# Performance work log

Measured on AMD Instinct MI355X. Metric: run time of the kernel, lower is better.

## Reference

```python
import jax, jax.numpy as jnp
import numpy as np

B, NQ, NK, C = 16, 8, 4096, 256
H = W = 64
HEADS = 8
CI = 128          # embedding_dim // attention_downsample_rate
HD = CI // HEADS  # per-head dim
EPS = float(np.finfo(np.float32).tiny)


def _gumbel_topk(scores, noise, n):
    # iterative gumbel-softmax top-k relaxation with straight-through hard k-hot
    g = scores + noise
    khot = jnp.zeros_like(g)
    onehot = jnp.zeros_like(g)
    for _ in range(n):
        g = g + jnp.log(jnp.maximum(1.0 - onehot, EPS))
        onehot = jax.nn.softmax(g, axis=-1)
        khot = khot + onehot
    _, ind = jax.lax.top_k(khot, n)
    rows = jnp.arange(khot.shape[0])[:, None]
    hard = jnp.zeros_like(khot).at[rows, ind].set(1.0)
    ret = hard - jax.lax.stop_gradient(khot) + khot  # == hard numerically
    return ret, jnp.sort(ind, axis=1)  # sorted idx = row-major order of boolean-mask select


def _sample_points(pe, content, ret, idx):
    # pe [H,W,C], content [b,H,W,C], ret [b,HW] k-hot, idx [b,k] sorted
    b = ret.shape[0]
    m = ret.reshape(b, H, W, 1)
    pe_m = (pe[None] * m).reshape(b, H * W, -1)
    c_m = (content * m).reshape(b, H * W, -1)
    take = lambda a: jnp.take_along_axis(a, idx[:, :, None], axis=1)
    return take(pe_m), take(c_m)


def _mlp(x, W1, b1, W2, b2, W3, b3):
    x = jax.nn.relu(x @ W1 + b1)
    x = jax.nn.relu(x @ W2 + b2)
    return x @ W3 + b3


def _forward(queries, keys, query_pe, key_pe, guiding_embedding, gumbel_p, gumbel_n,
             static_uncertain, static_refined, Wq, bq, Wk, bk, Wv, bv, Wo, bo,
             uW1, ub1, uW2, ub2, uW3, ub3, rW1, rb1, rW2, rb2, rW3, rb3,
             pe_gauss, point_pos, point_neg, n_sample_points):
    b = queries.shape[0]
    g = guiding_embedding.reshape(b, C, H * W).transpose(0, 2, 1)  # [b, HW, C]
    g = g * keys  # elementwise gating -> new guiding embedding

    # cross attention token -> image (internal dim CI, HEADS heads)
    def split_heads(x, Wx, bx):
        return (x @ Wx + bx).reshape(b, -1, HEADS, HD).transpose(0, 2, 1, 3)
    qh = split_heads(queries + query_pe, Wq, bq)
    kh = split_heads(g + key_pe, Wk, bk)
    vh = split_heads(g, Wv, bv)
    attn = jax.nn.softmax(jnp.einsum('bhqd,bhkd->bhqk', qh, kh) / np.float32(np.sqrt(HD)), axis=-1)
    out = jnp.einsum('bhqk,bhkd->bhqd', attn, vh).transpose(0, 2, 1, 3).reshape(b, -1, CI)
    queries = out @ Wo + bo  # [b, NQ, C]

    q1 = queries[:, 1, :]
    unc_tok = _mlp(jnp.concatenate([jnp.broadcast_to(static_uncertain, (b, C)), q1], -1),
                   uW1, ub1, uW2, ub2, uW3, ub3)
    ref_tok = _mlp(jnp.concatenate([jnp.broadcast_to(static_refined, (b, C)), q1], -1),
                   rW1, rb1, rW2, rb2, rW3, rb3)

    img = g.transpose(0, 2, 1)  # [b, C, HW]
    unc_norm = jax.nn.sigmoid(jnp.einsum('bc,bcn->bn', unc_tok, img))
    ref_mask = jnp.einsum('bc,bcn->bn', ref_tok, img)
    coarse_mask = jnp.einsum('bc,bcn->bn', q1, img)

    queries = jnp.concatenate([queries[:, 0:1], ref_tok[:, None, :], queries[:, 2:]], axis=1)

    # point-sampling reference map + gumbel-softmax top-k (training-path math)
    ref_map = unc_norm * (jax.nn.sigmoid(ref_mask) - jax.nn.sigmoid(coarse_mask))  # [b, HW]
    ret_p, idx_p = _gumbel_topk(ref_map, gumbel_p, n_sample_points)
    ret_n, idx_n = _gumbel_topk(-ref_map, gumbel_n, n_sample_points)

    # random fourier positional encoding of the 64x64 grid (SAM PositionEmbeddingRandom)
    xs = (jnp.arange(W, dtype=jnp.float32) + 0.5) / W
    ys = (jnp.arange(H, dtype=jnp.float32) + 0.5) / H
    coords = jnp.stack([jnp.tile(xs[None, :], (H, 1)), jnp.tile(ys[:, None], (1, W))], axis=-1)
    proj = ((2.0 * coords - 1.0) @ pe_gauss) * np.float32(2.0 * np.pi)  # [H, W, C//2]
    pe = jnp.concatenate([jnp.sin(proj), jnp.cos(proj)], axis=-1)       # [H, W, C]

    # F.interpolate of a 64x64 map to (64,64) is the identity here
    content = (keys + g).reshape(b, H, W, C)

    sp_pe, sp_c = _sample_points(pe, content, ret_p, idx_p)
    sn_pe, sn_c = _sample_points(pe, content, ret_n, idx_n)
    sp_pe = sp_pe + point_pos  # prompt_encoder.point_embeddings[1]
    sn_pe = sn_pe + point_neg  # prompt_encoder.point_embeddings[0]

    query_pe = jnp.concatenate([query_pe, sp_pe, sn_pe], axis=1)
    queries = jnp.concatenate([queries, sp_c, sn_c], axis=1)
    # pack (queries, query_pe) into one array for a single-output reference
    return jnp.concatenate([queries, query_pe], axis=1)  # [b, 2*(NQ+2k), C]


def setup_inputs():
    key = jax.random.key(0)
    ks = iter(jax.random.split(key, 48))
    n = lambda shape, s=1.0: jax.random.normal(next(ks), shape, jnp.float32) * s
    z = lambda shape: jnp.zeros(shape, jnp.float32)
    return {
        'queries': n((B, NQ, C)),
        'keys': n((B, NK, C)),
        'query_pe': n((B, NQ, C)),
        'key_pe': n((B, NK, C)),
        'guiding_embedding': n((B, C, H, W)),
        'gumbel_p': jax.random.gumbel(next(ks), (B, NK), jnp.float32),
        'gumbel_n': jax.random.gumbel(next(ks), (B, NK), jnp.float32),
        'static_uncertain': n((C,), 0.02),
        'static_refined': n((C,), 0.02),
        'Wq': n((C, CI), 0.02), 'bq': z((CI,)),
        'Wk': n((C, CI), 0.02), 'bk': z((CI,)),
        'Wv': n((C, CI), 0.02), 'bv': z((CI,)),
        'Wo': n((CI, C), 0.02), 'bo': z((C,)),
        'uW1': n((2 * C, C // 4), 0.05), 'ub1': z((C // 4,)),
        'uW2': n((C // 4, C // 4), 0.05), 'ub2': z((C // 4,)),
        'uW3': n((C // 4, C), 0.05), 'ub3': z((C,)),
        'rW1': n((2 * C, C // 4), 0.05), 'rb1': z((C // 4,)),
        'rW2': n((C // 4, C // 4), 0.05), 'rb2': z((C // 4,)),
        'rW3': n((C // 4, C), 0.05), 'rb3': z((C,)),
        'pe_gauss': n((2, C // 2)),
        'point_pos': n((C,), 0.02),
        'point_neg': n((C,), 0.02),
        'n_sample_points': 4,
    }


def reference(queries, keys, query_pe, key_pe, guiding_embedding, gumbel_p, gumbel_n,
              static_uncertain, static_refined, Wq, bq, Wk, bk, Wv, bv, Wo, bo,
              uW1, ub1, uW2, ub2, uW3, ub3, rW1, rb1, rW2, rb2, rW3, rb3,
              pe_gauss, point_pos, point_neg, n_sample_points):
    return _forward(queries, keys, query_pe, key_pe, guiding_embedding, gumbel_p, gumbel_n,
                    static_uncertain, static_refined, Wq, bq, Wk, bk, Wv, bv, Wo, bo,
                    uW1, ub1, uW2, ub2, uW3, ub3, rW1, rb1, rW2, rb2, rW3, rb3,
                    pe_gauss, point_pos, point_neg, n_sample_points)
```

## Files before the change

### kernel.cpp

```cpp
#include <hip/hip_runtime.h>

#define BB 16
#define NQn 8
#define NK 4096
#define CC 256
#define NHEADS 8
#define CIn 128
#define HDn 16
#define NHQ 64
#define EPS_TINY 1.17549435e-38f

constexpr size_t OFF_QK   = 0;
constexpr size_t OFF_QBK  = OFF_QK  + (size_t)BB*CC*NHQ;
constexpr size_t OFF_SC   = OFF_QBK + (size_t)BB*NHQ;
constexpr size_t OFF_MP   = OFF_SC  + (size_t)BB*NK*NHQ;
constexpr size_t OFF_SP   = OFF_MP  + (size_t)BB*64*NHQ;
constexpr size_t OFF_M    = OFF_SP  + (size_t)BB*64*NHQ;
constexpr size_t OFF_RS   = OFF_M   + (size_t)BB*NHQ;
constexpr size_t OFF_AVP  = OFF_RS  + (size_t)BB*NHQ;
constexpr size_t OFF_QATT = OFF_AVP + (size_t)BB*16*NHQ*CC;
constexpr size_t OFF_UNC  = OFF_QATT+ (size_t)BB*NQn*CC;
constexpr size_t OFF_REFT = OFF_UNC + (size_t)BB*CC;
constexpr size_t OFF_RMAP = OFF_REFT+ (size_t)BB*CC;
constexpr size_t OFF_IDX  = OFF_RMAP+ (size_t)BB*NK;
constexpr size_t OFF_RV   = OFF_IDX + 128;
constexpr size_t OFF_G    = OFF_RV  + 128;

__global__ __launch_bounds__(256) void k1_qside(
    const float* __restrict__ queries, const float* __restrict__ query_pe,
    const float* __restrict__ Wq, const float* __restrict__ bq,
    const float* __restrict__ Wk, const float* __restrict__ bk,
    float* __restrict__ ws)
{
  int b = blockIdx.x >> 3, q = blockIdx.x & 7, t = threadIdx.x;
  __shared__ float x[CC];
  __shared__ float qh[CIn];
  x[t] = queries[(b*NQn+q)*CC + t] + query_pe[(b*NQn+q)*CC + t];
  __syncthreads();
  if (t < CIn) {
    float a = bq[t];
    for (int c = 0; c < CC; ++c) a += x[c]*Wq[c*CIn + t];
    qh[t] = a * 0.25f;
  }
  __syncthreads();
  float* Qk = ws + OFF_QK;
  #pragma unroll
  for (int h = 0; h < NHEADS; ++h) {
    float a = 0.f;
    #pragma unroll
    for (int d = 0; d < HDn; ++d) a += qh[h*HDn+d] * Wk[t*CIn + h*HDn + d];
    Qk[((size_t)b*CC + t)*NHQ + h*NQn + q] = a;
  }
  if (t < NHEADS) {
    float a = 0.f;
    #pragma unroll
    for (int d = 0; d < HDn; ++d) a += qh[t*HDn+d] * bk[t*HDn+d];
    (ws + OFF_QBK)[b*NHQ + t*NQn + q] = a;
  }
}

__global__ __launch_bounds__(256, 4) void k2_scores(
    const float* __restrict__ keys, const float* __restrict__ key_pe,
    const float* __restrict__ guiding, float* __restrict__ ws)
{
  int b = blockIdx.y, blk = blockIdx.x, n0 = blk * 64, t = threadIdx.x;
  __shared__ __align__(16) float Xs[64][36];
  __shared__ __align__(16) float Qs[32][64];
  __shared__ float Gt[32][66];
  const float* Qk = ws + OFF_QK + (size_t)b*CC*NHQ;
  float* G = ws + OFF_G;
  const int tx = t & 15, ty = t >> 4;
  const int xr = t >> 2, xco = (t & 3) * 8;
  const int gr = (t >> 6) * 8, gn = t & 63;
  float acc[4][4] = {};

  float gld[8]; float4 k0v, k1v, p0v, p1v; float qp[8];
  {
    #pragma unroll
    for (int i = 0; i < 8; ++i)
      gld[i] = guiding[((size_t)b*CC + gr + i)*NK + n0 + gn];
    size_t kb = ((size_t)b*NK + n0 + xr)*CC + xco;
    k0v = *(const float4*)&keys[kb];   k1v = *(const float4*)&keys[kb+4];
    p0v = *(const float4*)&key_pe[kb]; p1v = *(const float4*)&key_pe[kb+4];
    #pragma unroll
    for (int i = 0; i < 8; ++i) {
      int l = i*256 + t;
      qp[i] = Qk[(size_t)(l>>6)*NHQ + (l & 63)];
    }
  }
  for (int ch = 0; ch < 8; ++ch) {
    int c0 = ch*32;
    #pragma unroll
    for (int i = 0; i < 8; ++i) Gt[gr + i][gn] = gld[i];
    __syncthreads();
    #pragma unroll
    for (int i = 0; i < 8; ++i) {
      int l = i*256 + t;
      Qs[l>>6][l&63] = qp[i];
    }
    {
      size_t kbase = ((size_t)b*NK + n0 + xr)*CC + c0 + xco;
      float4 g0, g1;
      g0.x = k0v.x * Gt[xco+0][xr]; g0.y = k0v.y * Gt[xco+1][xr];
      g0.z = k0v.z * Gt[xco+2][xr]; g0.w = k0v.w * Gt[xco+3][xr];
      g1.x = k1v.x * Gt[xco+4][xr]; g1.y = k1v.y * Gt[xco+5][xr];
      g1.z = k1v.z * Gt[xco+6][xr]; g1.w = k1v.w * Gt[xco+7][xr];
      *(float4*)&G[kbase]   = g0;
      *(float4*)&G[kbase+4] = g1;
      float4 x0, x1;
      x0.x = g0.x+p0v.x; x0.y = g0.y+p0v.y; x0.z = g0.z+p0v.z; x0.w = g0.w+p0v.w;
      x1.x = g1.x+p1v.x; x1.y = g1.y+p1v.y; x1.z = g1.z+p1v.z; x1.w = g1.w+p1v.w;
      *(float4*)&Xs[xr][xco]   = x0;
      *(float4*)&Xs[xr][xco+4] = x1;
    }
    __syncthreads();
    if (ch < 7) {
      int c1 = c0 + 32;
      #pragma unroll
      for (int i = 0; i < 8; ++i)
        gld[i] = guiding[((size_t)b*CC + c1 + gr + i)*NK + n0 + gn];
      size_t kb2 = ((size_t)b*NK + n0 + xr)*CC + c1 + xco;
      k0v = *(const float4*)&keys[kb2];   k1v = *(const float4*)&keys[kb2+4];
      p0v = *(const float4*)&key_pe[kb2]; p1v = *(const float4*)&key_pe[kb2+4];
      #pragma unroll
      for (int i = 0; i < 8; ++i) {
        int l = i*256 + t;
        qp[i] = Qk[(size_t)(c1 + (l>>6))*NHQ + (l & 63)];
      }
    }
    #pragma unroll 4
    for (int cb = 0; cb < 8; ++cb) {
      float4 xf[4];
      #pragma unroll
      for (int i = 0; i < 4; ++i) xf[i] = *(const float4*)&Xs[4*ty+i][4*cb];
      #pragma unroll
      for (int u = 0; u < 4; ++u) {
        float4 qf = *(const float4*)&Qs[4*cb+u][4*tx];
        float xu[4] = { ((const float*)&xf[0])[u], ((const float*)&xf[1])[u],
                        ((const float*)&xf[2])[u], ((const float*)&xf[3])[u] };
        #pragma unroll
        for (int i = 0; i < 4; ++i) {
          acc[i][0] += xu[i]*qf.x; acc[i][1] += xu[i]*qf.y;
          acc[i][2] += xu[i]*qf.z; acc[i][3] += xu[i]*qf.w;
        }
      }
    }
  }
  const float* qbk = ws + OFF_QBK + (size_t)b*NHQ;
  float qb[4] = {qbk[4*tx], qbk[4*tx+1], qbk[4*tx+2], qbk[4*tx+3]};
  float* scp = ws + OFF_SC + ((size_t)b*NK + n0)*NHQ;
  #pragma unroll
  for (int i = 0; i < 4; ++i) {
    acc[i][0] += qb[0]; acc[i][1] += qb[1]; acc[i][2] += qb[2]; acc[i][3] += qb[3];
    float4 o; o.x = acc[i][0]; o.y = acc[i][1]; o.z = acc[i][2]; o.w = acc[i][3];
    *(float4*)&scp[(size_t)(4*ty + i)*NHQ + 4*tx] = o;
  }
  __syncthreads();
  float* red  = &Qs[0][0];
  float* mfin = &Gt[0][0];
  #pragma unroll
  for (int j = 0; j < 4; ++j) {
    float lm = fmaxf(fmaxf(acc[0][j], acc[1][j]), fmaxf(acc[2][j], acc[3][j]));
    red[ty*64 + 4*tx + j] = lm;
  }
  __syncthreads();
  if (t < 64) {
    float m = red[t];
    #pragma unroll
    for (int r = 1; r < 16; ++r) m = fmaxf(m, red[r*64 + t]);
    mfin[t] = m;
  }
  __syncthreads();
  #pragma unroll
  for (int j = 0; j < 4; ++j) {
    float m = mfin[4*tx + j];
    float ls = expf(acc[0][j]-m) + expf(acc[1][j]-m) + expf(acc[2][j]-m) + expf(acc[3][j]-m);
    red[ty*64 + 4*tx + j] = ls;
  }
  __syncthreads();
  if (t < 64) {
    float s = 0.f;
    #pragma unroll
    for (int r = 0; r < 16; ++r) s += red[r*64 + t];
    (ws + OFF_MP)[((size_t)b*64 + blk)*NHQ + t] = mfin[t];
    (ws + OFF_SP)[((size_t)b*64 + blk)*NHQ + t] = s;
  }
}

__global__ __launch_bounds__(64) void k3b_combine(float* __restrict__ ws)
{
  int b = blockIdx.x, hq = threadIdx.x;
  const float* mp = ws + OFF_MP + (size_t)b*64*NHQ;
  const float* sp = ws + OFF_SP + (size_t)b*64*NHQ;
  float m = -INFINITY;
  #pragma unroll 8
  for (int i = 0; i < 64; ++i) m = fmaxf(m, mp[i*NHQ+hq]);
  float s = 0.f;
  #pragma unroll 8
  for (int i = 0; i < 64; ++i) s += sp[i*NHQ+hq]*expf(mp[i*NHQ+hq]-m);
  (ws+OFF_M)[b*NHQ+hq] = m;
  (ws+OFF_RS)[b*NHQ+hq] = 1.0f/s;
}

__global__ __launch_bounds__(512) void k4_av(float* __restrict__ ws)
{
  int kb = blockIdx.x, b = blockIdx.y, t = threadIdx.x;
  int k0 = kb * 256;
  int wv = t >> 6, lane = t & 63;
  int hqb = wv * 8, c0 = lane * 4;
  __shared__ __align__(16) float gld[32][260];
  __shared__ __align__(16) float wld[32][68];
  __shared__ float mv[64], rv[64];
  if (t < 64) { mv[t] = (ws+OFF_M)[b*NHQ+t]; rv[t] = (ws+OFF_RS)[b*NHQ+t]; }
  const float* scp = ws + OFF_SC;
  const float* G  = ws + OFF_G;
  const int sr = t >> 4, scb = (t & 15) * 4;
  float acc[8][4] = {};
  float4 gp[4]; float wp[4];
  #pragma unroll
  for (int p = 0; p < 4; ++p)
    gp[p] = *(const float4*)&G[((size_t)b*NK + k0 + sr)*CC + scb + p*64];
  #pragma unroll
  for (int i = 0; i < 4; ++i) {
    int l = i*512 + t;
    wp[i] = scp[((size_t)b*NK + k0 + (l>>6))*NHQ + (l&63)];
  }
  __syncthreads();
  for (int kk = 0; kk < 256; kk += 32) {
    #pragma unroll
    for (int p = 0; p < 4; ++p)
      *(float4*)&gld[sr][scb + p*64] = gp[p];
    #pragma unroll
    for (int i = 0; i < 4; ++i) {
      int l = i*512 + t; int k = l >> 6, hq = l & 63;
      wld[k][hq] = expf(wp[i] - mv[hq]) * rv[hq];
    }
    __syncthreads();
    if (kk + 32 < 256) {
      #pragma unroll
      for (int p = 0; p < 4; ++p)
        gp[p] = *(const float4*)&G[((size_t)b*NK + k0+kk+32 + sr)*CC + scb + p*64];
      #pragma unroll
      for (int i = 0; i < 4; ++i) {
        int l = i*512 + t;
        wp[i] = scp[((size_t)b*NK + k0+kk+32 + (l>>6))*NHQ + (l&63)];
      }
    }
    #pragma unroll 2
    for (int k = 0; k < 32; ++k) {
      float4 g4 = *(const float4*)&gld[k][c0];
      float4 w0 = *(const float4*)&wld[k][hqb];
      float4 w1 = *(const float4*)&wld[k][hqb+4];
      float wq[8] = {w0.x,w0.y,w0.z,w0.w, w1.x,w1.y,w1.z,w1.w};
      #pragma unroll
      for (int i = 0; i < 8; ++i) {
        acc[i][0] += wq[i]*g4.x; acc[i][1] += wq[i]*g4.y;
        acc[i][2] += wq[i]*g4.z; acc[i][3] += wq[i]*g4.w;
      }
    }
    __syncthreads();
  }
  float* avp = ws + OFF_AVP + (((size_t)b*16 + kb)*NHQ)*CC;
  #pragma unroll
  for (int i = 0; i < 8; ++i) {
    float4 o; o.x=acc[i][0]; o.y=acc[i][1]; o.z=acc[i][2]; o.w=acc[i][3];
    *(float4*)&avp[(size_t)(hqb + i)*CC + c0] = o;
  }
}

__global__ __launch_bounds__(256) void k56_attout(
    const float* __restrict__ Wv, const float* __restrict__ bv,
    const float* __restrict__ Wo, const float* __restrict__ bo,
    const float* __restrict__ su, const float* __restrict__ sr,
    const float* __restrict__ uW1, const float* __restrict__ ub1,
    const float* __restrict__ uW2, const float* __restrict__ ub2,
    const float* __restrict__ uW3, const float* __restrict__ ub3,
    const float* __restrict__ rW1, const float* __restrict__ rb1,
    const float* __restrict__ rW2, const float* __restrict__ rb2,
    const float* __restrict__ rW3, const float* __restrict__ rb3,
    float* __restrict__ ws)
{
  int b = blockIdx.x >> 3, q = blockIdx.x & 7, t = threadIdx.x;
  __shared__ float avs[NHEADS][CC];
  __shared__ float outv[CIn];
  __shared__ float xs[768];
  __shared__ float h1[2][64], h2[2][64];
  const float* avp = ws + OFF_AVP;
  #pragma unroll
  for (int h = 0; h < NHEADS; ++h) {
    int hq = h*NQn + q;
    float a = 0.f;
    #pragma unroll 4
    for (int kb = 0; kb < 16; ++kb)
      a += avp[(((size_t)b*16 + kb)*NHQ + hq)*CC + t];
    avs[h][t] = a;
  }
  __syncthreads();
  if (t < CIn) {
    int h = t >> 4;
    float a = bv[t];
    for (int c = 0; c < CC; ++c) a += avs[h][c]*Wv[c*CIn + t];
    outv[t] = a;
  }
  __syncthreads();
  float a = bo[t];
  for (int ci = 0; ci < CIn; ++ci) a += outv[ci]*Wo[ci*CC + t];
  (ws+OFF_QATT)[((size_t)b*NQn + q)*CC + t] = a;

  if (q != 1) return;
  xs[t] = su[t];
  xs[256+t] = a;
  xs[512+t] = sr[t];
  __syncthreads();
  if (t < 128) {
    int which = t >> 6, o = t & 63;
    const float* W1 = which ? rW1 : uW1;
    const float* b1 = which ? rb1 : ub1;
    int base = which ? 512 : 0;
    float acc1 = b1[o];
    for (int i = 0; i < 256; ++i) acc1 += xs[base+i]*W1[i*64 + o];
    for (int i = 0; i < 256; ++i) acc1 += xs[256+i]*W1[(256+i)*64 + o];
    h1[which][o] = fmaxf(acc1, 0.f);
  }
  __syncthreads();
  if (t < 128) {
    int which = t >> 6, o = t & 63;
    const float* W2 = which ? rW2 : uW2;
    const float* b2 = which ? rb2 : ub2;
    float acc2 = b2[o];
    #pragma unroll 8
    for (int i = 0; i < 64; ++i) acc2 += h1[which][i]*W2[i*64+o];
    h2[which][o] = fmaxf(acc2, 0.f);
  }
  __syncthreads();
  {
    float au = ub3[t];
    #pragma unroll 8
    for (int i = 0; i < 64; ++i) au += h2[0][i]*uW3[i*CC + t];
    (ws+OFF_UNC)[b*CC + t] = au;
    float ar = rb3[t];
    #pragma unroll 8
    for (int i = 0; i < 64; ++i) ar += h2[1][i]*rW3[i*CC + t];
    (ws+OFF_REFT)[b*CC + t] = ar;
  }
}

__global__ __launch_bounds__(256) void k8_masks(float* __restrict__ ws)
{
  int b = blockIdx.y, t = threadIdx.x;
  int wave = t >> 6, lane = t & 63;
  __shared__ float q1s[CC], us[CC], rts[CC];
  q1s[t] = (ws+OFF_QATT)[((size_t)b*NQn+1)*CC + t];
  us[t]  = (ws+OFF_UNC)[b*CC + t];
  rts[t] = (ws+OFF_REFT)[b*CC + t];
  __syncthreads();
  float q1v[4], usv[4], rtv[4];
  #pragma unroll
  for (int u = 0; u < 4; ++u) {
    q1v[u] = q1s[lane*4+u]; usv[u] = us[lane*4+u]; rtv[u] = rts[lane*4+u];
  }
  const float* G = ws + OFF_G;
  float* rmap = ws + OFF_RMAP + (size_t)b*NK;
  int n_base = blockIdx.x*32 + wave*8;
  for (int r = 0; r < 8; ++r) {
    int n = n_base + r;
    float4 gv = *(const float4*)&G[((size_t)b*NK + n)*CC + lane*4];
    float aq = gv.x*q1v[0] + gv.y*q1v[1] + gv.z*q1v[2] + gv.w*q1v[3];
    float au = gv.x*usv[0] + gv.y*usv[1] + gv.z*usv[2] + gv.w*usv[3];
    float ar = gv.x*rtv[0] + gv.y*rtv[1] + gv.z*rtv[2] + gv.w*rtv[3];
    #pragma unroll
    for (int s = 1; s < 64; s <<= 1) {
      aq += __shfl_xor(aq, s, 64);
      au += __shfl_xor(au, s, 64);
      ar += __shfl_xor(ar, s, 64);
    }
    if (lane == 0) {
      float un = 1.f/(1.f+expf(-au));
      rmap[n] = un * (1.f/(1.f+expf(-ar)) - 1.f/(1.f+expf(-aq)));
    }
  }
}

__global__ __launch_bounds__(512) void k9_gumbel(
    const float* __restrict__ gp, const float* __restrict__ gn,
    float* __restrict__ ws)
{
  int sign = blockIdx.x, b = blockIdx.y, t = threadIdx.x;
  int wave = t >> 6, lane = t & 63;
  const float* noise = sign ? gn : gp;
  const float* rmap = ws + OFF_RMAP + (size_t)b*NK;
  float g[8], kh[8], oh[8];
  #pragma unroll
  for (int i = 0; i < 8; ++i) {
    int n = i*512 + t;
    float scv = rmap[n];
    if (sign) scv = -scv;
    g[i] = scv + noise[(size_t)b*NK + n];
    kh[i] = 0.f; oh[i] = 0.f;
  }
  __shared__ float wred[16];
  __shared__ float selV[32];
  __shared__ int   selIdx[32];
  for (int it = 0; it < 4; ++it) {
    if (it > 0) {
      #pragma unroll
      for (int i = 0; i < 8; ++i) g[i] += logf(fmaxf(1.f - oh[i], EPS_TINY));
    }
    float m = g[0];
    #pragma unroll
    for (int i = 1; i < 8; ++i) m = fmaxf(m, g[i]);
    #pragma unroll
    for (int s = 1; s < 64; s <<= 1) m = fmaxf(m, __shfl_xor(m, s, 64));
    if (lane == 0) wred[wave] = m;
    __syncthreads();
    m = wred[0];
    #pragma unroll
    for (int w = 1; w < 8; ++w) m = fmaxf(m, wred[w]);
    float e[8], ls = 0.f;
    #pragma unroll
    for (int i = 0; i < 8; ++i) { e[i] = expf(g[i]-m); ls += e[i]; }
    #pragma unroll
    for (int s = 1; s < 64; s <<= 1) ls += __shfl_xor(ls, s, 64);
    if (lane == 0) wred[8+wave] = ls;
    __syncthreads();
    float ssum = wred[8];
    #pragma unroll
    for (int w = 1; w < 8; ++w) ssum += wred[8+w];
    #pragma unroll
    for (int i = 0; i < 8; ++i) { oh[i] = e[i]/ssum; kh[i] += oh[i]; }
  }
  int id[4]; float rr[4];
  for (int j = 0; j < 4; ++j) {
    float bv = kh[0]; int bi = t;
    #pragma unroll
    for (int i = 1; i < 8; ++i) {
      if (kh[i] > bv) { bv = kh[i]; bi = i*512 + t; }
    }
    #pragma unroll
    for (int s = 1; s < 64; s <<= 1) {
      float ov = __shfl_xor(bv, s, 64);
      int   oi = __shfl_xor(bi, s, 64);
      if (ov > bv || (ov == bv && oi < bi)) { bv = ov; bi = oi; }
    }
    if (lane == 0) { selV[j*8+wave] = bv; selIdx[j*8+wave] = bi; }
    __syncthreads();
    bv = selV[j*8]; bi = selIdx[j*8];
    #pragma unroll
    for (int w = 1; w < 8; ++w) {
      float ov = selV[j*8+w]; int oi = selIdx[j*8+w];
      if (ov > bv || (ov == bv && oi < bi)) { bv = ov; bi = oi; }
    }
    id[j] = bi; rr[j] = (1.f - bv) + bv;
    if ((bi & 511) == t) kh[bi >> 9] = -1.f;
  }
  if (t == 0) {
    for (int a = 0; a < 3; ++a)
      for (int c2 = a+1; c2 < 4; ++c2)
        if (id[c2] < id[a]) { int ti=id[a]; id[a]=id[c2]; id[c2]=ti; float tr=rr[a]; rr[a]=rr[c2]; rr[c2]=tr; }
    int* iout = (int*)(ws + OFF_IDX);
    float* rout = ws + OFF_RV;
    for (int j = 0; j < 4; ++j) {
      iout[(sign*BB + b)*4 + j] = id[j];
      rout[(sign*BB + b)*4 + j] = rr[j];
    }
  }
}

__global__ __launch_bounds__(256) void k10_out(
    const float* __restrict__ keys, const float* __restrict__ query_pe,
    const float* __restrict__ point_pos, const float* __restrict__ point_neg,
    const float* __restrict__ pe_gauss,
    float* __restrict__ ws, float* __restrict__ out)
{
  int b = blockIdx.y, r = blockIdx.x, t = threadIdx.x;
  const float* G = ws + OFF_G;
  float val;
  if (r < 8) {
    val = (r == 1) ? (ws+OFF_REFT)[b*CC + t]
                   : (ws+OFF_QATT)[((size_t)b*NQn + r)*CC + t];
  } else if (r < 16) {
    int j = r - 8; int sign = j >> 2; int jj = j & 3;
    int idx = ((const int*)(ws+OFF_IDX))[(sign*BB + b)*4 + jj];
    float rvv = (ws+OFF_RV)[(sign*BB + b)*4 + jj];
    float kv = keys[((size_t)b*NK + idx)*CC + t];
    float gv = G[((size_t)b*NK + idx)*CC + t];
    val = (kv + gv) * rvv;
  } else if (r < 24) {
    val = query_pe[((size_t)b*NQn + (r-16))*CC + t];
  } else {
    int j = r - 24; int sign = j >> 2; int jj = j & 3;
    int idx = ((const int*)(ws+OFF_IDX))[(sign*BB + b)*4 + jj];
    float rvv = (ws+OFF_RV)[(sign*BB + b)*4 + jj];
    const float* point = sign ? point_neg : point_pos;
    int h = idx >> 6, w = idx & 63;
    float x = (w + 0.5f)/64.f, y = (h + 0.5f)/64.f;
    int jf = (t < 128) ? t : (t - 128);
    float proj = ((2.f*x - 1.f)*pe_gauss[jf] + (2.f*y - 1.f)*pe_gauss[128 + jf]) * 6.28318530717958647692f;
    float sv = (t < 128) ? sinf(proj) : cosf(proj);
    val = sv*rvv + point[t];
  }
  out[((size_t)b*32 + r)*CC + t] = val;
}

extern "C" void kernel_launch(void* const* d_in, const int* in_sizes, int n_in,
                              void* d_out, int out_size, void* d_ws, size_t ws_size,
                              hipStream_t stream)
{
  const float* queries   = (const float*)d_in[0];
  const float* keys      = (const float*)d_in[1];
  const float* query_pe  = (const float*)d_in[2];
  const float* key_pe    = (const float*)d_in[3];
  const float* guiding   = (const float*)d_in[4];
  const float* gumbel_p  = (const float*)d_in[5];
  const float* gumbel_n  = (const float*)d_in[6];
  const float* s_unc     = (const float*)d_in[7];
  const float* s_ref     = (const float*)d_in[8];
  const float* Wq  = (const float*)d_in[9];   const float* bq  = (const float*)d_in[10];
  const float* Wk  = (const float*)d_in[11];  const float* bk  = (const float*)d_in[12];
  const float* Wv  = (const float*)d_in[13];  const float* bv  = (const float*)d_in[14];
  const float* Wo  = (const float*)d_in[15];  const float* bo  = (const float*)d_in[16];
  const float* uW1 = (const float*)d_in[17];  const float* ub1 = (const float*)d_in[18];
  const float* uW2 = (const float*)d_in[19];  const float* ub2 = (const float*)d_in[20];
  const float* uW3 = (const float*)d_in[21];  const float* ub3 = (const float*)d_in[22];
  const float* rW1 = (const float*)d_in[23];  const float* rb1 = (const float*)d_in[24];
  const float* rW2 = (const float*)d_in[25];  const float* rb2 = (const float*)d_in[26];
  const float* rW3 = (const float*)d_in[27];  const float* rb3 = (const float*)d_in[28];
  const float* pe_gauss  = (const float*)d_in[29];
  const float* point_pos = (const float*)d_in[30];
  const float* point_neg = (const float*)d_in[31];
  float* ws = (float*)d_ws;
  float* out = (float*)d_out;

  k1_qside  <<<dim3(BB*NQn),    256, 0, stream>>>(queries, query_pe, Wq, bq, Wk, bk, ws);
  k2_scores <<<dim3(64, BB),    256, 0, stream>>>(keys, key_pe, guiding, ws);
  k3b_combine<<<dim3(BB),        64, 0, stream>>>(ws);
  k4_av     <<<dim3(16, BB),    512, 0, stream>>>(ws);
  k56_attout<<<dim3(BB*NQn),    256, 0, stream>>>(Wv, bv, Wo, bo,
                                                  s_unc, s_ref,
                                                  uW1, ub1, uW2, ub2, uW3, ub3,
                                                  rW1, rb1, rW2, rb2, rW3, rb3, ws);
  k8_masks  <<<dim3(128, BB),   256, 0, stream>>>(ws);
  k9_gumbel <<<dim3(2, BB),     512, 0, stream>>>(gumbel_p, gumbel_n, ws);
  k10_out   <<<dim3(32, BB),    256, 0, stream>>>(keys, query_pe, point_pos, point_neg,
                                                  pe_gauss, ws, out);
}
```

Measured before the change: 232.5 us.

## Fuse softmax combine into AV kernel and split channels across more blocks

Removes the separate k3b_combine launch by having each AV block recompute the global max and reciprocal sum for its batch from the partial stats. The AV kernel is also re-tiled: the grid gains a channel-chunk dimension of 64 columns with 256 threads per block and a 4x4 per-thread tile, raising block count from 256 to 1024. The aim is to drop one launch and improve occupancy. The cost is redundant combine work in every block, recomputing exp weights four times across channel chunks, and losing the register prefetch double-buffering.

```diff
diff --git a/kernel.cpp b/kernel.cpp
--- a/kernel.cpp
+++ b/kernel.cpp
@@ -187,84 +187,61 @@
   }
 }
 
-__global__ __launch_bounds__(64) void k3b_combine(float* __restrict__ ws)
-{
-  int b = blockIdx.x, hq = threadIdx.x;
-  const float* mp = ws + OFF_MP + (size_t)b*64*NHQ;
-  const float* sp = ws + OFF_SP + (size_t)b*64*NHQ;
-  float m = -INFINITY;
-  #pragma unroll 8
-  for (int i = 0; i < 64; ++i) m = fmaxf(m, mp[i*NHQ+hq]);
-  float s = 0.f;
-  #pragma unroll 8
-  for (int i = 0; i < 64; ++i) s += sp[i*NHQ+hq]*expf(mp[i*NHQ+hq]-m);
-  (ws+OFF_M)[b*NHQ+hq] = m;
-  (ws+OFF_RS)[b*NHQ+hq] = 1.0f/s;
-}
-
-__global__ __launch_bounds__(512) void k4_av(float* __restrict__ ws)
-{
-  int kb = blockIdx.x, b = blockIdx.y, t = threadIdx.x;
-  int k0 = kb * 256;
-  int wv = t >> 6, lane = t & 63;
-  int hqb = wv * 8, c0 = lane * 4;
-  __shared__ __align__(16) float gld[32][260];
-  __shared__ __align__(16) float wld[32][68];
+__global__ __launch_bounds__(256) void k4_av(float* __restrict__ ws)
+{
+  int kb = blockIdx.x, ch = blockIdx.y, b = blockIdx.z, t = threadIdx.x;
+  int k0 = kb * 256, cbase = ch * 64;
+  __shared__ __align__(16) float gld[32][68];
+  __shared__ __align__(16) float wld[32][64];
   __shared__ float mv[64], rv[64];
-  if (t < 64) { mv[t] = (ws+OFF_M)[b*NHQ+t]; rv[t] = (ws+OFF_RS)[b*NHQ+t]; }
-  const float* scp = ws + OFF_SC;
+  if (t < 64) {
+    const float* mp = ws + OFF_MP + (size_t)b*64*NHQ;
+    const float* sp = ws + OFF_SP + (size_t)b*64*NHQ;
+    float m = -INFINITY;
+    #pragma unroll 8
+    for (int i = 0; i < 64; ++i) m = fmaxf(m, mp[i*NHQ+t]);
+    float s = 0.f;
+    #pragma unroll 8
+    for (int i = 0; i < 64; ++i) s += sp[i*NHQ+t]*expf(mp[i*NHQ+t]-m);
+    mv[t] = m; rv[t] = 1.0f/s;
+  }
+  int hq0 = (t & 15) * 4, c0 = (t >> 4) * 4;
+  int sr = t >> 4, sc4 = (t & 15) * 4;
+  float accf[4][4] = {};
+  const float* sc = ws + OFF_SC;
   const float* G  = ws + OFF_G;
-  const int sr = t >> 4, scb = (t & 15) * 4;
-  float acc[8][4] = {};
-  float4 gp[4]; float wp[4];
-  #pragma unroll
-  for (int p = 0; p < 4; ++p)
-    gp[p] = *(const float4*)&G[((size_t)b*NK + k0 + sr)*CC + scb + p*64];
+  __syncthreads();
+  for (int kk = 0; kk < 256; kk += 32) {
+    #pragma unroll
+    for (int p = 0; p < 2; ++p)
+      *(float4*)&gld[p*16 + sr][sc4] =
+        *(const float4*)&G[((size_t)b*NK + k0+kk + p*16 + sr)*CC + cbase + sc4];
+    #pragma unroll
+    for (int i = 0; i < 8; ++i) {
+      int l = i*256 + t; int k = l >> 6, hq = l & 63;
+      float v = sc[((size_t)b*NK + k0+kk+k)*NHQ + hq];
+      wld[k][hq] = expf(v - mv[hq]) * rv[hq];
+    }
+    __syncthreads();
+    #pragma unroll 4
+    for (int k = 0; k < 32; ++k) {
+      float4 w4 = *(const float4*)&wld[k][hq0];
+      float4 gv = *(const float4*)&gld[k][c0];
+      float wq[4] = {w4.x, w4.y, w4.z, w4.w};
+      float gq[4] = {gv.x, gv.y, gv.z, gv.w};
+      #pragma unroll
+      for (int i = 0; i < 4; ++i)
+        #pragma unroll
+        for (int j = 0; j < 4; ++j) accf[i][j] += wq[i]*gq[j];
+    }
+    __syncthreads();
+  }
+  float* avp = ws + OFF_AVP + (((size_t)b*16 + kb)*NHQ)*CC;
   #pragma unroll
   for (int i = 0; i < 4; ++i) {
-    int l = i*512 + t;
-    wp[i] = scp[((size_t)b*NK + k0 + (l>>6))*NHQ + (l&63)];
-  }
-  __syncthreads();
-  for (int kk = 0; kk < 256; kk += 32) {
-    #pragma unroll
-    for (int p = 0; p < 4; ++p)
-      *(float4*)&gld[sr][scb + p*64] = gp[p];
-    #pragma unroll
-    for (int i = 0; i < 4; ++i) {
-      int l = i*512 + t; int k = l >> 6, hq = l & 63;
-      wld[k][hq] = expf(wp[i] - mv[hq]) * rv[hq];
-    }
-    __syncthreads();
-    if (kk + 32 < 256) {
-      #pragma unroll
-      for (int p = 0; p < 4; ++p)
-        gp[p] = *(const float4*)&G[((size_t)b*NK + k0+kk+32 + sr)*CC + scb + p*64];
-      #pragma unroll
-      for (int i = 0; i < 4; ++i) {
-        int l = i*512 + t;
-        wp[i] = scp[((size_t)b*NK + k0+kk+32 + (l>>6))*NHQ + (l&63)];
-      }
-    }
-    #pragma unroll 2
-    for (int k = 0; k < 32; ++k) {
-      float4 g4 = *(const float4*)&gld[k][c0];
-      float4 w0 = *(const float4*)&wld[k][hqb];
-      float4 w1 = *(const float4*)&wld[k][hqb+4];
-      float wq[8] = {w0.x,w0.y,w0.z,w0.w, w1.x,w1.y,w1.z,w1.w};
-      #pragma unroll
-      for (int i = 0; i < 8; ++i) {
-        acc[i][0] += wq[i]*g4.x; acc[i][1] += wq[i]*g4.y;
-        acc[i][2] += wq[i]*g4.z; acc[i][3] += wq[i]*g4.w;
-      }
-    }
-    __syncthreads();
-  }
-  float* avp = ws + OFF_AVP + (((size_t)b*16 + kb)*NHQ)*CC;
-  #pragma unroll
-  for (int i = 0; i < 8; ++i) {
-    float4 o; o.x=acc[i][0]; o.y=acc[i][1]; o.z=acc[i][2]; o.w=acc[i][3];
-    *(float4*)&avp[(size_t)(hqb + i)*CC + c0] = o;
+    float4 o;
+    o.x = accf[i][0]; o.y = accf[i][1]; o.z = accf[i][2]; o.w = accf[i][3];
+    *(float4*)&avp[(size_t)(hq0 + i)*CC + cbase + c0] = o;
   }
 }
 
@@ -533,8 +510,7 @@
 
   k1_qside  <<<dim3(BB*NQn),    256, 0, stream>>>(queries, query_pe, Wq, bq, Wk, bk, ws);
   k2_scores <<<dim3(64, BB),    256, 0, stream>>>(keys, key_pe, guiding, ws);
-  k3b_combine<<<dim3(BB),        64, 0, stream>>>(ws);
-  k4_av     <<<dim3(16, BB),    512, 0, stream>>>(ws);
+  k4_av     <<<dim3(16, 4, BB), 256, 0, stream>>>(ws);
   k56_attout<<<dim3(BB*NQn),    256, 0, stream>>>(Wv, bv, Wo, bo,
                                                   s_unc, s_ref,
                                                   uW1, ub1, uW2, ub2, uW3, ub3,
```

Result: faster. 219.3 us (-5.7%).
